# Performance work log

Measured on AMD Instinct MI355X. Metric: run time of the kernel, lower is better.

## Reference

```python
import jax, jax.numpy as jnp
import numpy as np

V, E, Hd, ENC, A = 2000, 256, 256, 256, 256
B, HI, WI, T = 64, 16, 32, 256


def setup_inputs() -> dict:
    key = jax.random.key(0)
    ks = jax.random.split(key, 24)
    n = lambda k, s: jax.random.normal(k, s, dtype=jnp.float32) * 0.05
    return {
        "encoder_out": jax.random.normal(ks[0], (B, ENC, HI, WI), dtype=jnp.float32),
        "captions": jax.random.randint(ks[1], (B, T), 0, V),
        "emb": n(ks[2], (V, E)),
        "W_ae": n(ks[3], (A, ENC)), "b_ae": jnp.zeros((A,), jnp.float32),
        "W_ad": n(ks[4], (A, Hd)), "b_ad": jnp.zeros((A,), jnp.float32),
        "W_fa": n(ks[5], (1, A)), "b_fa": jnp.zeros((1,), jnp.float32),
        "W_inith": n(ks[6], (Hd, ENC)), "b_inith": jnp.zeros((Hd,), jnp.float32),
        "W_initc": n(ks[7], (Hd, ENC)), "b_initc": jnp.zeros((Hd,), jnp.float32),
        "W_ih0": n(ks[8], (4 * Hd, E + ENC)), "W_hh0": n(ks[9], (4 * Hd, Hd)),
        "b_ih0": jnp.zeros((4 * Hd,), jnp.float32), "b_hh0": jnp.zeros((4 * Hd,), jnp.float32),
        "W_ih1": n(ks[10], (4 * Hd, Hd)), "W_hh1": n(ks[11], (4 * Hd, Hd)),
        "b_ih1": jnp.zeros((4 * Hd,), jnp.float32), "b_hh1": jnp.zeros((4 * Hd,), jnp.float32),
        "W_out": n(ks[12], (V, Hd)), "b_out": jnp.zeros((V,), jnp.float32),
    }


def _lstm_cell(x, h, c, Wih, Whh, bih, bhh):
    # PyTorch LSTM gate order: i, f, g, o
    g = x @ Wih.T + h @ Whh.T + bih + bhh
    i, f, gg, o = jnp.split(g, 4, axis=-1)
    c2 = jax.nn.sigmoid(f) * c + jax.nn.sigmoid(i) * jnp.tanh(gg)
    h2 = jax.nn.sigmoid(o) * jnp.tanh(c2)
    return h2, c2


def reference(encoder_out, captions, emb, W_ae, b_ae, W_ad, b_ad, W_fa, b_fa,
              W_inith, b_inith, W_initc, b_initc,
              W_ih0, W_hh0, b_ih0, b_hh0, W_ih1, W_hh1, b_ih1, b_hh1,
              W_out, b_out):
    Bsz, C = encoder_out.shape[0], encoder_out.shape[1]
    enc = encoder_out.reshape(Bsz, C, -1).transpose(0, 2, 1)  # [B, P, C]
    mean = encoder_out.mean(axis=(2, 3))                      # [B, C]
    h0 = jnp.tanh(mean @ W_inith.T + b_inith)
    c0 = jnp.tanh(mean @ W_initc.T + b_initc)
    h = jnp.stack([h0, h0])  # [L, B, Hd]
    c = jnp.stack([c0, c0])
    embs = emb[captions]     # [B, T, E] (dropout disabled / eval)
    att1 = enc @ W_ae.T + b_ae  # [B, P, A], hoisted out of the loop (same math)

    def step(carry, e_t):
        h, c = carry
        att2 = h[-1] @ W_ad.T + b_ad                              # [B, A]
        score = (jnp.tanh(att1 + att2[:, None, :]) @ W_fa.T)[..., 0] + b_fa[0]  # [B, P]
        w = jax.nn.softmax(score, axis=1)
        ctx = jnp.einsum('bp,bpc->bc', w, enc)
        x = jnp.concatenate([e_t, ctx], axis=1)                   # [B, E+C]
        h0n, c0n = _lstm_cell(x, h[0], c[0], W_ih0, W_hh0, b_ih0, b_hh0)
        h1n, c1n = _lstm_cell(h0n, h[1], c[1], W_ih1, W_hh1, b_ih1, b_hh1)
        out_t = h1n @ W_out.T + b_out
        return (jnp.stack([h0n, h1n]), jnp.stack([c0n, c1n])), (out_t, w)

    _, (outs, ws) = jax.lax.scan(step, (h, c), embs.transpose(1, 0, 2))
    return outs.transpose(1, 0, 2), ws.transpose(1, 0, 2)  # [B,T,V], [B,T,P]
```

## Files before the change

### kernel.cpp

```cpp
#include <hip/hip_runtime.h>
#include <math.h>

#define BB 64
#define TT 256
#define VV 2000
#define EE 256
#define HD 256
#define ENC 256
#define AA 256
#define PP 512

#define S2L 2.8853900817779268f
#define SL  1.4426950408889634f


typedef unsigned uvec4 __attribute__((ext_vector_type(4)));

__device__ __forceinline__ unsigned short f2h(float f) {
    _Float16 h = (_Float16)f; return __builtin_bit_cast(unsigned short, h);
}
__device__ __forceinline__ void fmlo(float& a, unsigned w, float x) {
    asm("v_fma_mix_f32 %0, %1, %2, %0 op_sel_hi:[1,0,0]" : "+v"(a) : "v"(w), "v"(x));
}
__device__ __forceinline__ void fmhi(float& a, unsigned w, float x) {
    asm("v_fma_mix_f32 %0, %1, %2, %0 op_sel:[1,0,0] op_sel_hi:[1,0,0]" : "+v"(a) : "v"(w), "v"(x));
}
__device__ __forceinline__ void dot8m(float& a0, float& a1, uvec4 w, float4 xa, float4 xb) {
    fmlo(a0, w.x, xa.x); fmhi(a1, w.x, xa.y);
    fmlo(a0, w.y, xa.z); fmhi(a1, w.y, xa.w);
    fmlo(a0, w.z, xb.x); fmhi(a1, w.z, xb.y);
    fmlo(a0, w.w, xb.z); fmhi(a1, w.w, xb.w);
}
__device__ __forceinline__ void dot8s(float& a, uvec4 w, const float* x) {
    fmlo(a, w.x, x[0]); fmhi(a, w.x, x[1]);
    fmlo(a, w.y, x[2]); fmhi(a, w.y, x[3]);
    fmlo(a, w.z, x[4]); fmhi(a, w.z, x[5]);
    fmlo(a, w.w, x[6]); fmhi(a, w.w, x[7]);
}
__device__ __forceinline__ float ftanh(float x) {
    float u = __builtin_amdgcn_exp2f(x * S2L);
    return 1.f - 2.f * __builtin_amdgcn_rcpf(u + 1.f);
}
__device__ __forceinline__ float fsigm(float x) {
    float u = __builtin_amdgcn_exp2f(x * SL);
    return u * __builtin_amdgcn_rcpf(u + 1.f);
}


__global__ void k_mean(const float* __restrict__ enc, float* __restrict__ meanb) {
    int b = blockIdx.x, c = threadIdx.x;
    const float4* p4 = reinterpret_cast<const float4*>(enc + ((size_t)b*ENC + c)*PP);
    float s = 0.f;
    for (int i = 0; i < PP/4; ++i) { float4 v = p4[i]; s += v.x + v.y + v.z + v.w; }
    meanb[b*ENC + c] = s * (1.0f/PP);
}

__global__ void k_init(const float* __restrict__ meanb,
                       const float* __restrict__ Winith, const float* __restrict__ binith,
                       const float* __restrict__ Winitc, const float* __restrict__ binitc,
                       float* __restrict__ h0, float* __restrict__ c0,
                       float* __restrict__ h1i, float* __restrict__ c1) {
    __shared__ float ms[ENC];
    int b = blockIdx.x, j = threadIdx.x;
    ms[j] = meanb[b*ENC + j];
    __syncthreads();
    float ah = binith[j], ac = binitc[j];
    const float4* wh = (const float4*)(Winith + (size_t)j*ENC);
    const float4* wc = (const float4*)(Winitc + (size_t)j*ENC);
    const float4* m4 = (const float4*)ms;
    for (int k = 0; k < ENC/4; ++k) {
        float4 m = m4[k], a = wh[k], b2 = wc[k];
        ah += a.x*m.x + a.y*m.y + a.z*m.z + a.w*m.w;
        ac += b2.x*m.x + b2.y*m.y + b2.z*m.z + b2.w*m.w;
    }
    float hv = tanhf(ah), cv = tanhf(ac);
    h0[b*HD + j] = hv; c0[b*HD + j] = cv;
    h1i[b*HD + j] = hv; c1[b*HD + j] = cv;
}

__global__ void k_att1T8(const float* __restrict__ enc, const float* __restrict__ Wae,
                         const float* __restrict__ bae, unsigned short* __restrict__ att1T8) {
    __shared__ float wsm[16][ENC];
    int a0 = blockIdx.x * 16, b = blockIdx.y, p = threadIdx.x;
    for (int i = threadIdx.x; i < 16*ENC; i += 512) wsm[i >> 8][i & 255] = Wae[(size_t)a0*ENC + i];
    __syncthreads();
    float acc[16];
    #pragma unroll
    for (int i = 0; i < 16; ++i) acc[i] = 0.f;
    const float* eb = enc + (size_t)b*ENC*PP + p;
    for (int c = 0; c < ENC; ++c) {
        float v = eb[(size_t)c*PP];
        #pragma unroll
        for (int i = 0; i < 16; ++i) acc[i] += v * wsm[i][c];
    }
    #pragma unroll
    for (int q = 0; q < 2; ++q) {
        unsigned short o[8];
        #pragma unroll
        for (int j = 0; j < 8; ++j) o[j] = f2h((acc[q*8+j] + bae[a0 + q*8 + j]) * S2L);
        *(uint4*)(att1T8 + (((size_t)b*32 + (a0 >> 3) + q)*PP + p)*8) = *(const uint4*)o;
    }
}

__global__ void k_encP(const float* __restrict__ enc, unsigned short* __restrict__ encP) {
    __shared__ float tile[256*33];
    int b = blockIdx.x, p0 = blockIdx.y * 32, tid = threadIdx.x;
    for (int i = tid; i < 256*32; i += 256) {
        int c = i >> 5, pl = i & 31;
        tile[c*33 + pl] = enc[((size_t)b*ENC + c)*PP + p0 + pl];
    }
    __syncthreads();
    for (int j = tid; j < 32*256; j += 256) {
        int p = j >> 8, c = j & 255;
        encP[((size_t)b*PP + p0 + p)*ENC + c] = f2h(tile[c*33 + p]);
    }
}

__global__ void k_cvtT8(const float* __restrict__ src, unsigned short* __restrict__ dst,
                        int nsh, int kc, float scale) {
    int i = blockIdx.x*256 + threadIdx.x;
    int N = 1 << nsh;
    int kk = i >> nsh, n = i & (N - 1);
    const float* s = src + (size_t)n*(kc*8) + kk*8;
    unsigned short o[8];
    #pragma unroll
    for (int j = 0; j < 8; ++j) o[j] = f2h(s[j] * scale);
    *(uint4*)(dst + ((size_t)kk*N + n)*8) = *(const uint4*)o;
}

__global__ __launch_bounds__(1024) void k_E(const int* __restrict__ caps,
                                            const float* __restrict__ emb,
                                            const unsigned short* __restrict__ Wih0T8,
                                            unsigned short* __restrict__ E) {
    __shared__ float xs[16][256];
    __shared__ int cp[16];
    int b = blockIdx.x, tc = blockIdx.y, tid = threadIdx.x;
    if (tid < 16) cp[tid] = caps[b*TT + tc*16 + tid];
    __syncthreads();
    for (int i = tid; i < 16*256; i += 1024) {
        int r = i >> 8, c = i & 255;
        xs[r][c] = emb[(size_t)cp[r]*EE + c];
    }
    __syncthreads();
    const uvec4* wt = (const uvec4*)Wih0T8;
    float acc[16];
    #pragma unroll
    for (int r = 0; r < 16; ++r) acc[r] = 0.f;
    for (int kk = 0; kk < 32; ++kk) {
        uvec4 w = wt[(size_t)kk*1024 + tid];
        #pragma unroll
        for (int r = 0; r < 16; ++r) dot8s(acc[r], w, &xs[r][kk*8]);
    }
    #pragma unroll
    for (int r = 0; r < 16; ++r)
        E[((size_t)(b*TT + tc*16 + r))*1024 + tid] = f2h(acc[r]);
}


struct KP2 {
    const int* caps; const float* emb;
    const float* Wfa; const float* bfa; const float* bad;
    const float* bih0; const float* bhh0; const float* bih1; const float* bhh1;
    const unsigned short* WadT8;
    const unsigned short* Wih0T8;
    const unsigned short* Whh0T8;
    const unsigned short* Wih1T8;
    const unsigned short* Whh1T8;
    const unsigned short* att1T8;
    const unsigned short* encP;
    const unsigned short* E;
    const float* h0g; const float* c0g; const float* h1g; const float* c1g;
    float* H1all; float* wsout;
};

template <int USEE>
__global__ __launch_bounds__(1024, 1) void main64(KP2 P) {
    __shared__ float att2s[AA];
    __shared__ float xt[512];
    __shared__ float h0s[HD], h1s[HD];
    __shared__ float es[PP];
    __shared__ float red[2048];
    __shared__ float bs0[1024], bs1[1024];
    __shared__ float badS[AA], wfaS[AA];
    __shared__ float zinvS, bfaS, wfaSumS;

    const int b = blockIdx.x, tid = threadIdx.x;

    bs0[tid] = P.bih0[tid] + P.bhh0[tid];
    bs1[tid] = P.bih1[tid] + P.bhh1[tid];
    float c0r = 0.f, c1r = 0.f;
    if (tid < 256) {
        badS[tid] = P.bad[tid] * S2L;
        wfaS[tid] = P.Wfa[tid] * SL;
        h0s[tid] = P.h0g[b*HD + tid]; h1s[tid] = P.h1g[b*HD + tid];
        c0r = P.c0g[b*HD + tid];      c1r = P.c1g[b*HD + tid];
    }
    if (tid == 0) bfaS = P.bfa[0] * SL;
    __syncthreads();
    if (tid == 0) {
        float s = 0.f;
        for (int i = 0; i < 256; ++i) s += wfaS[i];
        wfaSumS = s;
    }
    __syncthreads();

    const int p_sc = tid & 511, h_sc = tid >> 9;
    const uvec4* att1b = (const uvec4*)(P.att1T8 + (size_t)b*32*PP*8) + (size_t)(h_sc*16)*PP + p_sc;
    const unsigned short* Eb = P.E + (size_t)b*TT*1024;
    const unsigned* encPb = (const unsigned*)(P.encP + (size_t)b*PP*ENC);
    const uvec4* wadt = (const uvec4*)P.WadT8;
    const uvec4* wi0t = (const uvec4*)P.Wih0T8;
    const uvec4* wh0t = (const uvec4*)P.Whh0T8;
    const uvec4* wi1t = (const uvec4*)P.Wih1T8;
    const uvec4* wh1t = (const uvec4*)P.Whh1T8;

    for (int t = 0; t < TT; ++t) {
        {
            int a = tid & 255, kq = tid >> 8;
            const uvec4* w4 = wadt + (size_t)(kq*8)*256 + a;
            const float4* hv = (const float4*)h1s;
            float a0 = 0.f, a1 = 0.f;
            #pragma unroll
            for (int i = 0; i < 8; ++i) {
                uvec4 w = w4[(size_t)i*256];
                dot8m(a0, a1, w, hv[(kq*8 + i)*2], hv[(kq*8 + i)*2 + 1]);
            }
            red[kq*256 + a] = a0 + a1;
        }
        if (!USEE && tid < 256) {
            int cap = P.caps[b*TT + t];
            xt[tid] = P.emb[(size_t)cap*EE + tid];
        }
        __syncthreads();
        if (tid < 256) att2s[tid] = red[tid] + red[256+tid] + red[512+tid] + red[768+tid] + badS[tid];
        __syncthreads();

        {
            float partial = 0.f;
            #pragma unroll 4
            for (int i = 0; i < 16; ++i) {
                uvec4 w = __builtin_nontemporal_load(att1b + (size_t)i*PP);
                int ab = (h_sc*16 + i)*8;
                #pragma unroll
                for (int j = 0; j < 4; ++j) {
                    unsigned wj = w[j];
                    float a2l = att2s[ab + j*2], a2h = att2s[ab + j*2 + 1];
                    float x0, x1;
                    asm("v_fma_mix_f32 %0, %1, %2, %3 op_sel_hi:[1,0,0]"
                        : "=v"(x0) : "v"(wj), "v"(1.0f), "v"(a2l));
                    asm("v_fma_mix_f32 %0, %1, %2, %3 op_sel:[1,0,0] op_sel_hi:[1,0,0]"
                        : "=v"(x1) : "v"(wj), "v"(1.0f), "v"(a2h));
                    float r0 = __builtin_amdgcn_rcpf(__builtin_amdgcn_exp2f(x0) + 1.f);
                    float r1 = __builtin_amdgcn_rcpf(__builtin_amdgcn_exp2f(x1) + 1.f);
                    partial = fmaf(wfaS[ab + j*2],     r0, partial);
                    partial = fmaf(wfaS[ab + j*2 + 1], r1, partial);
                }
            }
            red[h_sc*512 + p_sc] = partial;
        }
        __syncthreads();
        if (tid < 512)
            es[tid] = __builtin_amdgcn_exp2f(wfaSumS - 2.f*(red[tid] + red[512 + tid]) + bfaS);
        __syncthreads();

        if (tid < 64) {
            float z = 0.f;
            #pragma unroll
            for (int i = 0; i < 8; ++i) z += es[tid*8 + i];
            for (int o = 32; o > 0; o >>= 1) z += __shfl_down(z, o, 64);
            if (tid == 0) zinvS = 1.f / z;
        }
        {
            int c2 = tid & 127, pq = tid >> 7;
            float a0 = 0.f, a1 = 0.f;
            #pragma unroll 8
            for (int i = 0; i < 64; ++i) {
                int p = pq*64 + i;
                unsigned w = __builtin_nontemporal_load(encPb + (size_t)p*128 + c2);
                float e = es[p];
                fmlo(a0, w, e); fmhi(a1, w, e);
            }
            red[pq*256 + c2*2]     = a0;
            red[pq*256 + c2*2 + 1] = a1;
        }
        __syncthreads();
        if (tid < 256) {
            float s = 0.f;
            #pragma unroll
            for (int q = 0; q < 8; ++q) s += red[q*256 + tid];
            xt[256 + tid] = s * zinvS;
        } else if (tid >= 512) {
            int p = tid - 512;
            P.wsout[((size_t)b*TT + t)*PP + p] = es[p] * zinvS;
        }
        __syncthreads();

        {
            float a0 = bs0[tid], a1 = 0.f;
            if (USEE) {
                unsigned short eu = Eb[(size_t)t*1024 + tid];
                a0 += (float)__builtin_bit_cast(_Float16, eu);
            }
            const uvec4* wi = wi0t + tid;
            const float4* xv = (const float4*)xt;
            if (USEE) {
                #pragma unroll 8
                for (int kk = 32; kk < 64; ++kk) {
                    uvec4 w = wi[(size_t)kk*1024];
                    dot8m(a0, a1, w, xv[kk*2], xv[kk*2 + 1]);
                }
            } else {
                #pragma unroll 8
                for (int kk = 0; kk < 64; ++kk) {
                    uvec4 w = wi[(size_t)kk*1024];
                    dot8m(a0, a1, w, xv[kk*2], xv[kk*2 + 1]);
                }
            }
            const uvec4* wh = wh0t + tid;
            const float4* hv = (const float4*)h0s;
            #pragma unroll 8
            for (int kk = 0; kk < 32; ++kk) {
                uvec4 w = wh[(size_t)kk*1024];
                dot8m(a0, a1, w, hv[kk*2], hv[kk*2 + 1]);
            }
            red[tid] = a0 + a1;
        }
        __syncthreads();
        if (tid < 256) {
            float gi = red[tid], gf = red[HD+tid], gg = red[2*HD+tid], go = red[3*HD+tid];
            c0r = fsigm(gf)*c0r + fsigm(gi)*ftanh(gg);
            h0s[tid] = fsigm(go)*ftanh(c0r);
        }
        __syncthreads();

        {
            float a0 = bs1[tid], a1 = 0.f;
            const uvec4* wi = wi1t + tid;
            const float4* hv0 = (const float4*)h0s;
            #pragma unroll 8
            for (int kk = 0; kk < 32; ++kk) {
                uvec4 w = wi[(size_t)kk*1024];
                dot8m(a0, a1, w, hv0[kk*2], hv0[kk*2 + 1]);
            }
            const uvec4* wh = wh1t + tid;
            const float4* hv1 = (const float4*)h1s;
            #pragma unroll 8
            for (int kk = 0; kk < 32; ++kk) {
                uvec4 w = wh[(size_t)kk*1024];
                dot8m(a0, a1, w, hv1[kk*2], hv1[kk*2 + 1]);
            }
            red[tid] = a0 + a1;
        }
        __syncthreads();
        if (tid < 256) {
            float gi = red[tid], gf = red[HD+tid], gg = red[2*HD+tid], go = red[3*HD+tid];
            c1r = fsigm(gf)*c1r + fsigm(gi)*ftanh(gg);
            float h = fsigm(go)*ftanh(c1r);
            h1s[tid] = h;
            P.H1all[((size_t)t*BB + b)*HD + tid] = h;
        }
        __syncthreads();
    }
}


__global__ __launch_bounds__(256)
void f2_out(const float* __restrict__ H1all, const float* __restrict__ Wout,
            const float* __restrict__ bout, float* __restrict__ out0) {
    __shared__ float Hs[16][260];
    int vt = blockIdx.x, rt = blockIdx.y, tid = threadIdx.x;
    int r0 = rt * 16;
    for (int i = tid; i < 16*256; i += 256) {
        int rl = i >> 8, c = i & 255;
        Hs[rl][c] = H1all[(size_t)(r0 + rl)*HD + c];
    }
    __syncthreads();
    int r_l = tid & 15, v_l = tid >> 4;
    int r = r0 + r_l; int tt = r >> 6, bb2 = r & 63;
    float* orow = out0 + ((size_t)bb2*TT + tt)*VV;
    const float4* hs = (const float4*)Hs[r_l];
    int vbase = vt*128 + v_l*8;
    for (int i = 0; i < 8; ++i) {
        int v = vbase + i;
        if (v >= VV) break;
        const float4* wr = (const float4*)(Wout + (size_t)v*HD);
        float accA = 0.f, accB = 0.f;
        #pragma unroll 4
        for (int k = 0; k < 64; k += 2) {
            float4 w0 = wr[k],   h0 = hs[k];
            float4 w1 = wr[k+1], h1 = hs[k+1];
            accA += w0.x*h0.x + w0.y*h0.y + w0.z*h0.z + w0.w*h0.w;
            accB += w1.x*h1.x + w1.y*h1.y + w1.z*h1.z + w1.w*h1.w;
        }
        orow[v] = accA + accB + bout[v];
    }
}


extern "C" void kernel_launch(void* const* d_in, const int* in_sizes, int n_in,
                              void* d_out, int out_size, void* d_ws, size_t ws_size,
                              hipStream_t stream) {
    const float* enc    = (const float*)d_in[0];
    const int*   caps   = (const int*)  d_in[1];
    const float* emb    = (const float*)d_in[2];
    const float* Wae    = (const float*)d_in[3];
    const float* bae    = (const float*)d_in[4];
    const float* Wad    = (const float*)d_in[5];
    const float* bad    = (const float*)d_in[6];
    const float* Wfa    = (const float*)d_in[7];
    const float* bfa    = (const float*)d_in[8];
    const float* Winith = (const float*)d_in[9];
    const float* binith = (const float*)d_in[10];
    const float* Winitc = (const float*)d_in[11];
    const float* binitc = (const float*)d_in[12];
    const float* Wih0   = (const float*)d_in[13];
    const float* Whh0   = (const float*)d_in[14];
    const float* bih0   = (const float*)d_in[15];
    const float* bhh0   = (const float*)d_in[16];
    const float* Wih1   = (const float*)d_in[17];
    const float* Whh1   = (const float*)d_in[18];
    const float* bih1   = (const float*)d_in[19];
    const float* bhh1   = (const float*)d_in[20];
    const float* Wout   = (const float*)d_in[21];
    const float* bout   = (const float*)d_in[22];

    float* ws = (float*)d_ws;
    unsigned short* att1T8 = (unsigned short*)(ws);
    unsigned short* encP   = (unsigned short*)(ws + 4194304);
    float* H1all = ws + 8388608;
    unsigned short* Wih0T8 = (unsigned short*)(ws + 12582912);
    unsigned short* Whh0T8 = (unsigned short*)(ws + 12845056);
    unsigned short* Wih1T8 = (unsigned short*)(ws + 12976128);
    unsigned short* Whh1T8 = (unsigned short*)(ws + 13107200);
    unsigned short* WadT8  = (unsigned short*)(ws + 13238272);
    float* meanb = ws + 13271040;
    float* h0g   = ws + 13287424;
    float* c0g   = ws + 13303808;
    float* h1g   = ws + 13320192;
    float* c1g   = ws + 13336576;
    unsigned short* E = (unsigned short*)(ws + 13352960);

    const int useE = (ws_size >= (size_t)(13352960 + 8388608) * 4) ? 1 : 0;

    float* out0  = (float*)d_out;
    float* wsout = out0 + (size_t)BB*TT*VV;

    hipLaunchKernelGGL(k_mean,   dim3(BB),     dim3(256), 0, stream, enc, meanb);
    hipLaunchKernelGGL(k_init,   dim3(BB),     dim3(256), 0, stream, meanb, Winith, binith,
                       Winitc, binitc, h0g, c0g, h1g, c1g);
    hipLaunchKernelGGL(k_att1T8, dim3(16, BB), dim3(512), 0, stream, enc, Wae, bae, att1T8);
    hipLaunchKernelGGL(k_encP,   dim3(BB, 16), dim3(256), 0, stream, enc, encP);
    hipLaunchKernelGGL(k_cvtT8,  dim3(256),    dim3(256), 0, stream, Wih0, Wih0T8, 10, 64, 1.0f);
    hipLaunchKernelGGL(k_cvtT8,  dim3(128),    dim3(256), 0, stream, Whh0, Whh0T8, 10, 32, 1.0f);
    hipLaunchKernelGGL(k_cvtT8,  dim3(128),    dim3(256), 0, stream, Wih1, Wih1T8, 10, 32, 1.0f);
    hipLaunchKernelGGL(k_cvtT8,  dim3(128),    dim3(256), 0, stream, Whh1, Whh1T8, 10, 32, 1.0f);
    hipLaunchKernelGGL(k_cvtT8,  dim3(32),     dim3(256), 0, stream, Wad,  WadT8,   8, 32, S2L);
    if (useE)
        hipLaunchKernelGGL(k_E,  dim3(BB, 16), dim3(1024), 0, stream, caps, emb, Wih0T8, E);

    KP2 kp;
    kp.caps = caps; kp.emb = emb;
    kp.Wfa = Wfa; kp.bfa = bfa; kp.bad = bad;
    kp.bih0 = bih0; kp.bhh0 = bhh0; kp.bih1 = bih1; kp.bhh1 = bhh1;
    kp.WadT8 = WadT8; kp.Wih0T8 = Wih0T8; kp.Whh0T8 = Whh0T8; kp.Wih1T8 = Wih1T8; kp.Whh1T8 = Whh1T8;
    kp.att1T8 = att1T8; kp.encP = encP; kp.E = E;
    kp.h0g = h0g; kp.c0g = c0g; kp.h1g = h1g; kp.c1g = c1g;
    kp.H1all = H1all; kp.wsout = wsout;

    if (useE)
        hipLaunchKernelGGL((main64<1>), dim3(BB), dim3(1024), 0, stream, kp);
    else
        hipLaunchKernelGGL((main64<0>), dim3(BB), dim3(1024), 0, stream, kp);

    hipLaunchKernelGGL(f2_out, dim3(16, 1024), dim3(256), 0, stream, H1all, Wout, bout, out0);
}
```

Measured before the change: 10.57 ms.

## Rewrite output projection with fp16 transposed weights and register-blocked rows; prefetch encP

Adds a conversion of W_out to a packed fp16, k-major layout, and rewrites the output projection so each thread owns one vocabulary column and accumulates 32 rows in registers, reusing each weight load across those rows. It also prefetches the first half of the encoder context loads into registers before the attention-score loop, so their latency overlaps with the score computation. The costs are more register pressure in the main recurrent kernel, fp16 rounding of W_out, and reuse of the att1 buffer for the converted weights when workspace is small.

```diff
diff --git a/kernel.cpp b/kernel.cpp
--- a/kernel.cpp
+++ b/kernel.cpp
@@ -126,6 +126,18 @@
     #pragma unroll
     for (int j = 0; j < 8; ++j) o[j] = f2h(s[j] * scale);
     *(uint4*)(dst + ((size_t)kk*N + n)*8) = *(const uint4*)o;
+}
+
+__global__ void k_cvtW(const float* __restrict__ src, unsigned short* __restrict__ dst) {
+    int i = blockIdx.x*256 + threadIdx.x;
+    int kk = i >> 11, v = i & 2047;
+    unsigned short o[8] = {0,0,0,0,0,0,0,0};
+    if (v < VV) {
+        const float* s = src + (size_t)v*HD + kk*8;
+        #pragma unroll
+        for (int j = 0; j < 8; ++j) o[j] = f2h(s[j]);
+    }
+    *(uint4*)(dst + ((size_t)kk*2048 + v)*8) = *(const uint4*)o;
 }
 
 __global__ __launch_bounds__(1024) void k_E(const int* __restrict__ caps,
@@ -205,6 +217,7 @@
     __syncthreads();
 
     const int p_sc = tid & 511, h_sc = tid >> 9;
+    const int c2 = tid & 127, pq = tid >> 7;
     const uvec4* att1b = (const uvec4*)(P.att1T8 + (size_t)b*32*PP*8) + (size_t)(h_sc*16)*PP + p_sc;
     const unsigned short* Eb = P.E + (size_t)b*TT*1024;
     const unsigned* encPb = (const unsigned*)(P.encP + (size_t)b*PP*ENC);
@@ -235,7 +248,12 @@
         if (tid < 256) att2s[tid] = red[tid] + red[256+tid] + red[512+tid] + red[768+tid] + badS[tid];
         __syncthreads();
 
+        unsigned ew[32];
         {
+            #pragma unroll
+            for (int i = 0; i < 32; ++i)
+                ew[i] = __builtin_nontemporal_load(encPb + (size_t)(pq*64 + i)*128 + c2);
+
             float partial = 0.f;
             #pragma unroll 4
             for (int i = 0; i < 16; ++i) {
@@ -271,14 +289,17 @@
             if (tid == 0) zinvS = 1.f / z;
         }
         {
-            int c2 = tid & 127, pq = tid >> 7;
             float a0 = 0.f, a1 = 0.f;
+            #pragma unroll
+            for (int i = 0; i < 32; ++i) {
+                float e = es[pq*64 + i];
+                fmlo(a0, ew[i], e); fmhi(a1, ew[i], e);
+            }
             #pragma unroll 8
-            for (int i = 0; i < 64; ++i) {
-                int p = pq*64 + i;
-                unsigned w = __builtin_nontemporal_load(encPb + (size_t)p*128 + c2);
-                float e = es[p];
-                fmlo(a0, w, e); fmhi(a1, w, e);
+            for (int i = 32; i < 64; ++i) {
+                unsigned w2 = __builtin_nontemporal_load(encPb + (size_t)(pq*64 + i)*128 + c2);
+                float e = es[pq*64 + i];
+                fmlo(a0, w2, e); fmhi(a1, w2, e);
             }
             red[pq*256 + c2*2]     = a0;
             red[pq*256 + c2*2 + 1] = a1;
@@ -365,34 +386,27 @@
 
 
 __global__ __launch_bounds__(256)
-void f2_out(const float* __restrict__ H1all, const float* __restrict__ Wout,
-            const float* __restrict__ bout, float* __restrict__ out0) {
-    __shared__ float Hs[16][260];
+void f2o(const float* __restrict__ H1all, const unsigned short* __restrict__ WoT8,
+         const float* __restrict__ bout, float* __restrict__ out0) {
     int vt = blockIdx.x, rt = blockIdx.y, tid = threadIdx.x;
-    int r0 = rt * 16;
-    for (int i = tid; i < 16*256; i += 256) {
-        int rl = i >> 8, c = i & 255;
-        Hs[rl][c] = H1all[(size_t)(r0 + rl)*HD + c];
-    }
-    __syncthreads();
-    int r_l = tid & 15, v_l = tid >> 4;
-    int r = r0 + r_l; int tt = r >> 6, bb2 = r & 63;
-    float* orow = out0 + ((size_t)bb2*TT + tt)*VV;
-    const float4* hs = (const float4*)Hs[r_l];
-    int vbase = vt*128 + v_l*8;
-    for (int i = 0; i < 8; ++i) {
-        int v = vbase + i;
-        if (v >= VV) break;
-        const float4* wr = (const float4*)(Wout + (size_t)v*HD);
-        float accA = 0.f, accB = 0.f;
-        #pragma unroll 4
-        for (int k = 0; k < 64; k += 2) {
-            float4 w0 = wr[k],   h0 = hs[k];
-            float4 w1 = wr[k+1], h1 = hs[k+1];
-            accA += w0.x*h0.x + w0.y*h0.y + w0.z*h0.z + w0.w*h0.w;
-            accB += w1.x*h1.x + w1.y*h1.y + w1.z*h1.z + w1.w*h1.w;
-        }
-        orow[v] = accA + accB + bout[v];
+    int v = vt*256 + tid;
+    const float* Hrow = H1all + (size_t)rt*32*HD;
+    const uvec4* wt = (const uvec4*)WoT8;
+    float acc[32];
+    #pragma unroll
+    for (int r = 0; r < 32; ++r) acc[r] = 0.f;
+    for (int kk = 0; kk < 32; ++kk) {
+        uvec4 w = wt[(size_t)kk*2048 + v];
+        #pragma unroll
+        for (int r = 0; r < 32; ++r) dot8s(acc[r], w, Hrow + r*HD + kk*8);
+    }
+    if (v < VV) {
+        float bv = bout[v];
+        #pragma unroll
+        for (int r = 0; r < 32; ++r) {
+            int row = rt*32 + r, tt = row >> 6, bb = row & 63;
+            out0[((size_t)bb*TT + tt)*VV + v] = acc[r] + bv;
+        }
     }
 }
 
@@ -441,6 +455,9 @@
     unsigned short* E = (unsigned short*)(ws + 13352960);
 
     const int useE = (ws_size >= (size_t)(13352960 + 8388608) * 4) ? 1 : 0;
+    const int useWtail = (ws_size >= (size_t)(13352960 + 8388608 + 262144) * 4) ? 1 : 0;
+    unsigned short* WoT8 = useWtail ? (unsigned short*)(ws + 13352960 + 8388608)
+                                    : att1T8;
 
     float* out0  = (float*)d_out;
     float* wsout = out0 + (size_t)BB*TT*VV;
@@ -457,6 +474,8 @@
     hipLaunchKernelGGL(k_cvtT8,  dim3(32),     dim3(256), 0, stream, Wad,  WadT8,   8, 32, S2L);
     if (useE)
         hipLaunchKernelGGL(k_E,  dim3(BB, 16), dim3(1024), 0, stream, caps, emb, Wih0T8, E);
+    if (useWtail)
+        hipLaunchKernelGGL(k_cvtW, dim3(256),  dim3(256), 0, stream, Wout, WoT8);
 
     KP2 kp;
     kp.caps = caps; kp.emb = emb;
@@ -472,5 +491,8 @@
     else
         hipLaunchKernelGGL((main64<0>), dim3(BB), dim3(1024), 0, stream, kp);
 
-    hipLaunchKernelGGL(f2_out, dim3(16, 1024), dim3(256), 0, stream, H1all, Wout, bout, out0);
-}
+    if (!useWtail)
+        hipLaunchKernelGGL(k_cvtW, dim3(256),  dim3(256), 0, stream, Wout, WoT8);
+
+    hipLaunchKernelGGL(f2o, dim3(8, 512), dim3(256), 0, stream, H1all, WoT8, bout, out0);
+}
```

Result: slower. 11.76 ms (+11.2%).
